# Kernel optimization log

Hardware: AMD Instinct MI355X
Metric: run time of the kernel (lower is better)

## Reference

```python
import jax, jax.numpy as jnp
import numpy as np

H = 1024
NH = 16
HD = H // NH
EPS = 1e-5


def setup_inputs() -> dict:
    key = jax.random.key(0)
    ks = jax.random.split(key, 16)
    B, LQ, LK = 2, 1024, 2048
    s = 1.0 / np.sqrt(H)
    inp = {
        "query": jax.random.normal(ks[0], (B, LQ, H), jnp.float32),
        "key": jax.random.normal(ks[1], (B, LK, H), jnp.float32),
        "value": jax.random.normal(ks[2], (B, LK, H), jnp.float32),
        "mask": jax.random.randint(ks[3], (B, LQ, LK), 0, 2, jnp.int32),
        "Wq": jax.random.normal(ks[4], (H, H), jnp.float32) * s,
        "bq": jnp.zeros((H,), jnp.float32),
        "Wk": jax.random.normal(ks[5], (H, H), jnp.float32) * s,
        "bk": jnp.zeros((H,), jnp.float32),
        "Wv": jax.random.normal(ks[6], (H, H), jnp.float32) * s,
        "bv": jnp.zeros((H,), jnp.float32),
        "Wo": jax.random.normal(ks[7], (H, H), jnp.float32) * s,
        "bo": jnp.zeros((H,), jnp.float32),
        "ln_g": jnp.ones((H,), jnp.float32),
        "ln_b": jnp.zeros((H,), jnp.float32),
    }
    return inp


def _split_heads(x, B, L):
    # [B, L, H] -> [B, NH, L, HD]
    return x.reshape(B, L, NH, HD).transpose(0, 2, 1, 3)


def reference(query, key, value, mask, Wq, bq, Wk, bk, Wv, bv, Wo, bo, ln_g, ln_b):
    B, LQ, _ = query.shape
    LK = key.shape[1]
    # projections (torch Linear: x @ W.T + b)
    Q = _split_heads(query @ Wq.T + bq, B, LQ)   # [B,NH,LQ,HD]
    K = _split_heads(key   @ Wk.T + bk, B, LK)   # [B,NH,LK,HD]
    V = _split_heads(value @ Wv.T + bv, B, LK)   # [B,NH,LK,HD]
    scores = jnp.einsum('bhqd,bhkd->bhqk', Q, K) / np.sqrt(HD)
    scores = jnp.where(mask[:, None, :, :] == 0, jnp.float32(-1e9), scores)
    attn = jax.nn.softmax(scores, axis=-1)
    # dropout is identity in eval mode
    ctx = jnp.einsum('bhqk,bhkd->bhqd', attn, V)            # [B,NH,LQ,HD]
    ctx = ctx.transpose(0, 2, 1, 3).reshape(B, LQ, H)       # [B,LQ,H]
    out = ctx @ Wo.T + bo
    x = out + query
    mu = jnp.mean(x, axis=-1, keepdims=True)
    var = jnp.mean(jnp.square(x - mu), axis=-1, keepdims=True)
    return (x - mu) / jnp.sqrt(var + EPS) * ln_g + ln_b
```

## Files before the change

### kernel.cpp

```cpp
#include <hip/hip_runtime.h>
#include <hip/hip_bf16.h>

typedef __hip_bfloat16 hbf16;

#define Hdim 1024
#define NHEAD 16
#define HDIM 64
#define BATCH 2
#define LQ 1024
#define LK 2048
#define LN_EPS 1e-5f

typedef __bf16 bfv8 __attribute__((ext_vector_type(8)));
typedef float floatx4 __attribute__((ext_vector_type(4)));
typedef union { bfv8 v; __bf16 b[8]; unsigned short s[8]; } bfu8;

#define BK 32
#define LDS_PITCH 40
#define QT 64
#define KT 64
#define KS_PITCH 72
#define VT_OFF(d) ((d) * 72 + (((d) >> 3) << 3))
#define PS_OFF(r) ((r) * 72 + (((r) >> 2) << 3))

__device__ inline bfv8 cvt2(const float4 x, const float4 y) {
    bfv8 r = {(__bf16)x.x, (__bf16)x.y, (__bf16)x.z, (__bf16)x.w,
              (__bf16)y.x, (__bf16)y.y, (__bf16)y.z, (__bf16)y.w};
    return r;
}

__device__ __forceinline__ void glds16(const void* g, void* l) {
    __builtin_amdgcn_global_load_lds(
        (const __attribute__((address_space(1))) void*)g,
        (__attribute__((address_space(3))) void*)l, 16, 0, 0);
}

__global__ __launch_bounds__(256) void cvt_all(
    const float* __restrict__ q, const float* __restrict__ k,
    const float* __restrict__ v, const float* __restrict__ Wq,
    const float* __restrict__ Wk, const float* __restrict__ Wv,
    hbf16* __restrict__ qb, hbf16* __restrict__ kb, hbf16* __restrict__ vb,
    hbf16* __restrict__ Wqb, hbf16* __restrict__ Wkb, hbf16* __restrict__ Wvb) {
    const int blk = blockIdx.x;
    const float* src; hbf16* dst; int base;
    if (blk < 1024)      { src = q;  dst = qb;  base = blk; }
    else if (blk < 3072) { src = k;  dst = kb;  base = blk - 1024; }
    else if (blk < 5120) { src = v;  dst = vb;  base = blk - 3072; }
    else if (blk < 5632) { src = Wq; dst = Wqb; base = blk - 5120; }
    else if (blk < 6144) { src = Wk; dst = Wkb; base = blk - 5632; }
    else                 { src = Wv; dst = Wvb; base = blk - 6144; }
    const size_t e = (size_t)base * 2048 + (size_t)threadIdx.x * 8;
    const float4 a = *(const float4*)(src + e);
    const float4 b = *(const float4*)(src + e + 4);
    *(bfv8*)((__bf16*)dst + e) = cvt2(a, b);
}

__global__ __launch_bounds__(256) void proj3_glds(
    const hbf16* __restrict__ qb, const hbf16* __restrict__ kb,
    const hbf16* __restrict__ vb,
    const hbf16* __restrict__ Wqb, const hbf16* __restrict__ Wkb,
    const hbf16* __restrict__ Wvb,
    const float* __restrict__ bq, const float* __restrict__ bk,
    const float* __restrict__ bv,
    hbf16* __restrict__ Qp, hbf16* __restrict__ Kp, hbf16* __restrict__ Vp) {
    const int z = blockIdx.z;
    if (z == 0 && blockIdx.y >= (BATCH * LQ) / 128) return;
    const hbf16* A; const hbf16* W; const float* bias; hbf16* out; float scale;
    if (z == 0)      { A = qb; W = Wqb; bias = bq; out = Qp; scale = 0.125f; }
    else if (z == 1) { A = kb; W = Wkb; bias = bk; out = Kp; scale = 1.0f; }
    else             { A = vb; W = Wvb; bias = bv; out = Vp; scale = 1.0f; }

    __shared__ __align__(16) __bf16 As[2][128 * 32];
    __shared__ __align__(16) __bf16 Bs[2][128 * 32];
    const int tid = threadIdx.x;
    const int lane = tid & 63;
    const int w = tid >> 6;
    const int wm = w & 1, wn = w >> 1;
    const int u = lane & 15;
    const int quad = lane >> 4;
    const int rowBase = blockIdx.y * 128;
    const int colBase = blockIdx.x * 128;

    const int srow = tid >> 2;
    const int scol = (tid & 3) * 8;
    const hbf16* aP = A + (size_t)(rowBase + srow) * Hdim + scol;
    const hbf16* wP = W + (size_t)(colBase + srow) * Hdim + scol;
    const int ldsOff = srow * 32 + scol;

#define P_STAGE(buf, k0)                                            \
    do {                                                            \
        glds16(aP + (k0), &As[buf][ldsOff]);                        \
        glds16(aP + (k0) + (size_t)64 * Hdim, &As[buf][ldsOff + 64 * 32]); \
        glds16(wP + (k0), &Bs[buf][ldsOff]);                        \
        glds16(wP + (k0) + (size_t)64 * Hdim, &Bs[buf][ldsOff + 64 * 32]); \
    } while (0)

    floatx4 acc[4][4];
#pragma unroll
    for (int mi = 0; mi < 4; ++mi)
#pragma unroll
        for (int ni = 0; ni < 4; ++ni) acc[mi][ni] = (floatx4){0.f, 0.f, 0.f, 0.f};

#define P_COMPUTE(buf)                                                         \
    do {                                                                       \
        bfv8 af[4], bf[4];                                                     \
        _Pragma("unroll") for (int mi = 0; mi < 4; ++mi)                       \
            af[mi] = *(const bfv8*)&As[buf][(wm * 64 + mi * 16 + u) * 32 + quad * 8]; \
        _Pragma("unroll") for (int ni = 0; ni < 4; ++ni)                       \
            bf[ni] = *(const bfv8*)&Bs[buf][(wn * 64 + ni * 16 + u) * 32 + quad * 8]; \
        _Pragma("unroll") for (int mi = 0; mi < 4; ++mi)                       \
            _Pragma("unroll") for (int ni = 0; ni < 4; ++ni)                   \
                acc[mi][ni] = __builtin_amdgcn_mfma_f32_16x16x32_bf16(af[mi], bf[ni], acc[mi][ni], 0, 0, 0); \
    } while (0)

    P_STAGE(0, 0);
    __syncthreads();

    for (int t = 0; t < 32; t += 2) {
        if (t + 1 < 32) P_STAGE(1, (t + 1) * 32);
        P_COMPUTE(0);
        __syncthreads();
        if (t + 2 < 32) P_STAGE(0, (t + 2) * 32);
        P_COMPUTE(1);
        __syncthreads();
    }
#undef P_STAGE
#undef P_COMPUTE

#pragma unroll
    for (int mi = 0; mi < 4; ++mi)
#pragma unroll
        for (int ni = 0; ni < 4; ++ni) {
            const int n = colBase + wn * 64 + ni * 16 + u;
            const float bn = bias[n];
#pragma unroll
            for (int rr = 0; rr < 4; ++rr) {
                const int m = rowBase + wm * 64 + mi * 16 + quad * 4 + rr;
                out[(size_t)m * Hdim + n] = __float2bfloat16((acc[mi][ni][rr] + bn) * scale);
            }
        }
}

__global__ __launch_bounds__(256) void gemm_ctx2(const hbf16* __restrict__ A,
                                                 const float* __restrict__ W,
                                                 const float* __restrict__ bias,
                                                 const float* __restrict__ resid,
                                                 float* __restrict__ out) {
    __shared__ __align__(16) __bf16 As[2][64 * 32];
    __shared__ __align__(16) __bf16 Bs[2][64 * 32];
    const int tid = threadIdx.x;
    const int lane = tid & 63;
    const int w = tid >> 6;
    const int wm = w & 1, wn = w >> 1;
    const int u = lane & 15;
    const int quad = lane >> 4;
    const int rowBase = blockIdx.y * 64;
    const int colBase = blockIdx.x * 64;

    const int srow = tid >> 2;
    const int scol = (tid & 3) * 8;
    const hbf16* aP = A + (size_t)(rowBase + srow) * Hdim + scol;
    const int ldsOffA = srow * 32 + scol;

    const float* wP = W + (size_t)(colBase + srow) * Hdim + scol;
    const int ldsOffB = ldsOffA;

    floatx4 acc[2][2];
#pragma unroll
    for (int mi = 0; mi < 2; ++mi)
#pragma unroll
        for (int ni = 0; ni < 2; ++ni) acc[mi][ni] = (floatx4){0.f, 0.f, 0.f, 0.f};

#define C_COMPUTE(buf)                                                         \
    do {                                                                       \
        bfv8 af[2], bf[2];                                                     \
        _Pragma("unroll") for (int mi = 0; mi < 2; ++mi)                       \
            af[mi] = *(const bfv8*)&As[buf][(wm * 32 + mi * 16 + u) * 32 + quad * 8]; \
        _Pragma("unroll") for (int ni = 0; ni < 2; ++ni)                       \
            bf[ni] = *(const bfv8*)&Bs[buf][(wn * 32 + ni * 16 + u) * 32 + quad * 8]; \
        _Pragma("unroll") for (int mi = 0; mi < 2; ++mi)                       \
            _Pragma("unroll") for (int ni = 0; ni < 2; ++ni)                   \
                acc[mi][ni] = __builtin_amdgcn_mfma_f32_16x16x32_bf16(af[mi], bf[ni], acc[mi][ni], 0, 0, 0); \
    } while (0)

    {
        glds16(aP, &As[0][ldsOffA]);
        const float4* w4 = (const float4*)wP;
        const float4 w0 = w4[0], w1 = w4[1];
        *(bfv8*)&Bs[0][ldsOffB] = cvt2(w0, w1);
    }
    __syncthreads();

    for (int t = 0; t < 32; t += 2) {
        {
            float4 w0, w1;
            const bool pf = (t + 1 < 32);
            if (pf) {
                glds16(aP + (t + 1) * 32, &As[1][ldsOffA]);
                const float4* w4 = (const float4*)(wP + (t + 1) * 32);
                w0 = w4[0]; w1 = w4[1];
            }
            C_COMPUTE(0);
            if (pf) {
                *(bfv8*)&Bs[1][ldsOffB] = cvt2(w0, w1);
            }
            __syncthreads();
        }
        {
            float4 w0, w1;
            const bool pf = (t + 2 < 32);
            if (pf) {
                glds16(aP + (t + 2) * 32, &As[0][ldsOffA]);
                const float4* w4 = (const float4*)(wP + (t + 2) * 32);
                w0 = w4[0]; w1 = w4[1];
            }
            C_COMPUTE(1);
            if (pf) {
                *(bfv8*)&Bs[0][ldsOffB] = cvt2(w0, w1);
            }
            __syncthreads();
        }
    }
#undef C_COMPUTE

#pragma unroll
    for (int mi = 0; mi < 2; ++mi)
#pragma unroll
        for (int ni = 0; ni < 2; ++ni) {
            const int n = colBase + wn * 32 + ni * 16 + u;
            const float bn = bias[n];
#pragma unroll
            for (int rr = 0; rr < 4; ++rr) {
                const int m = rowBase + wm * 32 + mi * 16 + quad * 4 + rr;
                out[(size_t)m * Hdim + n] = acc[mi][ni][rr] + bn + resid[(size_t)m * Hdim + n];
            }
        }
}

__global__ __launch_bounds__(256) void proj3_mfma(
    const float* __restrict__ q_in, const float* __restrict__ k_in,
    const float* __restrict__ v_in,
    const float* __restrict__ Wq, const float* __restrict__ bq,
    const float* __restrict__ Wk, const float* __restrict__ bk,
    const float* __restrict__ Wv, const float* __restrict__ bv,
    hbf16* __restrict__ Qp, hbf16* __restrict__ Kp, hbf16* __restrict__ Vp) {
    const int z = blockIdx.z;
    if (z == 0 && blockIdx.y >= (BATCH * LQ) / 64) return;
    const float* A; const float* W; const float* bias; hbf16* out; float scale;
    if (z == 0)      { A = q_in; W = Wq; bias = bq; out = Qp; scale = 0.125f; }
    else if (z == 1) { A = k_in; W = Wk; bias = bk; out = Kp; scale = 1.0f; }
    else             { A = v_in; W = Wv; bias = bv; out = Vp; scale = 1.0f; }

    __shared__ __align__(16) __bf16 As[64 * LDS_PITCH];
    __shared__ __align__(16) __bf16 Bs[64 * LDS_PITCH];
    const int tid = threadIdx.x;
    const int lane = tid & 63;
    const int w = tid >> 6;
    const int wm = w & 1, wn = w >> 1;
    const int rowBase = blockIdx.y * 64;
    const int colBase = blockIdx.x * 64;
    const int sr = tid >> 2;
    const int scg = (tid & 3) * 8;
    const int lr = lane & 15;
    const int quad = lane >> 4;

    floatx4 acc[2][2] = {};

    for (int k0 = 0; k0 < Hdim; k0 += BK) {
        const float* ap = A + (size_t)(rowBase + sr) * Hdim + k0 + scg;
        bfv8 av = cvt2(((const float4*)ap)[0], ((const float4*)ap)[1]);
        const float* wp = W + (size_t)(colBase + sr) * Hdim + k0 + scg;
        bfv8 bv8 = cvt2(((const float4*)wp)[0], ((const float4*)wp)[1]);
        __syncthreads();
        *(bfv8*)&As[sr * LDS_PITCH + scg] = av;
        *(bfv8*)&Bs[sr * LDS_PITCH + scg] = bv8;
        __syncthreads();

        bfv8 bf[2];
#pragma unroll
        for (int nt = 0; nt < 2; ++nt)
            bf[nt] = *(const bfv8*)&Bs[(wn * 32 + nt * 16 + lr) * LDS_PITCH + quad * 8];
#pragma unroll
        for (int mt = 0; mt < 2; ++mt) {
            bfv8 af = *(const bfv8*)&As[(wm * 32 + mt * 16 + lr) * LDS_PITCH + quad * 8];
#pragma unroll
            for (int nt = 0; nt < 2; ++nt)
                acc[mt][nt] = __builtin_amdgcn_mfma_f32_16x16x32_bf16(af, bf[nt], acc[mt][nt], 0, 0, 0);
        }
    }

#pragma unroll
    for (int mt = 0; mt < 2; ++mt)
#pragma unroll
        for (int nt = 0; nt < 2; ++nt) {
            const int n = colBase + wn * 32 + nt * 16 + lr;
            const float bn = bias[n];
#pragma unroll
            for (int rr = 0; rr < 4; ++rr) {
                const int m = rowBase + wm * 32 + mt * 16 + quad * 4 + rr;
                out[(size_t)m * Hdim + n] = __float2bfloat16((acc[mt][nt][rr] + bn) * scale);
            }
        }
}

__global__ __launch_bounds__(256) void gemm_mfma_f32(const float* __restrict__ A,
                                                     const float* __restrict__ W,
                                                     const float* __restrict__ bias,
                                                     hbf16* __restrict__ out,
                                                     float scale) {
    __shared__ __align__(16) __bf16 As[64 * LDS_PITCH];
    __shared__ __align__(16) __bf16 Bs[64 * LDS_PITCH];
    const int tid = threadIdx.x;
    const int lane = tid & 63;
    const int w = tid >> 6;
    const int wm = w & 1, wn = w >> 1;
    const int rowBase = blockIdx.y * 64;
    const int colBase = blockIdx.x * 64;
    const int sr = tid >> 2;
    const int scg = (tid & 3) * 8;
    const int lr = lane & 15;
    const int quad = lane >> 4;

    floatx4 acc[2][2] = {};

    for (int k0 = 0; k0 < Hdim; k0 += BK) {
        const float* ap = A + (size_t)(rowBase + sr) * Hdim + k0 + scg;
        bfv8 av = cvt2(((const float4*)ap)[0], ((const float4*)ap)[1]);
        const float* wp = W + (size_t)(colBase + sr) * Hdim + k0 + scg;
        bfv8 bv = cvt2(((const float4*)wp)[0], ((const float4*)wp)[1]);
        __syncthreads();
        *(bfv8*)&As[sr * LDS_PITCH + scg] = av;
        *(bfv8*)&Bs[sr * LDS_PITCH + scg] = bv;
        __syncthreads();

        bfv8 bf[2];
#pragma unroll
        for (int nt = 0; nt < 2; ++nt)
            bf[nt] = *(const bfv8*)&Bs[(wn * 32 + nt * 16 + lr) * LDS_PITCH + quad * 8];
#pragma unroll
        for (int mt = 0; mt < 2; ++mt) {
            bfv8 af = *(const bfv8*)&As[(wm * 32 + mt * 16 + lr) * LDS_PITCH + quad * 8];
#pragma unroll
            for (int nt = 0; nt < 2; ++nt)
                acc[mt][nt] = __builtin_amdgcn_mfma_f32_16x16x32_bf16(af, bf[nt], acc[mt][nt], 0, 0, 0);
        }
    }

#pragma unroll
    for (int mt = 0; mt < 2; ++mt)
#pragma unroll
        for (int nt = 0; nt < 2; ++nt) {
            const int n = colBase + wn * 32 + nt * 16 + lr;
            const float bn = bias[n];
#pragma unroll
            for (int rr = 0; rr < 4; ++rr) {
                const int m = rowBase + wm * 32 + mt * 16 + quad * 4 + rr;
                out[(size_t)m * Hdim + n] = __float2bfloat16((acc[mt][nt][rr] + bn) * scale);
            }
        }
}

__global__ __launch_bounds__(256) void gemm_mfma_ctx(const hbf16* __restrict__ A,
                                                     const float* __restrict__ W,
                                                     const float* __restrict__ bias,
                                                     const float* __restrict__ resid,
                                                     float* __restrict__ out) {
    __shared__ __align__(16) __bf16 As[64 * LDS_PITCH];
    __shared__ __align__(16) __bf16 Bs[64 * LDS_PITCH];
    const int tid = threadIdx.x;
    const int lane = tid & 63;
    const int w = tid >> 6;
    const int wm = w & 1, wn = w >> 1;
    const int rowBase = blockIdx.y * 64;
    const int colBase = blockIdx.x * 64;
    const int sr = tid >> 2;
    const int scg = (tid & 3) * 8;
    const int lr = lane & 15;
    const int quad = lane >> 4;

    floatx4 acc[2][2] = {};

    for (int k0 = 0; k0 < Hdim; k0 += BK) {
        bfv8 av = *(const bfv8*)(A + (size_t)(rowBase + sr) * Hdim + k0 + scg);
        const float* wp = W + (size_t)(colBase + sr) * Hdim + k0 + scg;
        bfv8 bv = cvt2(((const float4*)wp)[0], ((const float4*)wp)[1]);
        __syncthreads();
        *(bfv8*)&As[sr * LDS_PITCH + scg] = av;
        *(bfv8*)&Bs[sr * LDS_PITCH + scg] = bv;
        __syncthreads();

        bfv8 bf[2];
#pragma unroll
        for (int nt = 0; nt < 2; ++nt)
            bf[nt] = *(const bfv8*)&Bs[(wn * 32 + nt * 16 + lr) * LDS_PITCH + quad * 8];
#pragma unroll
        for (int mt = 0; mt < 2; ++mt) {
            bfv8 af = *(const bfv8*)&As[(wm * 32 + mt * 16 + lr) * LDS_PITCH + quad * 8];
#pragma unroll
            for (int nt = 0; nt < 2; ++nt)
                acc[mt][nt] = __builtin_amdgcn_mfma_f32_16x16x32_bf16(af, bf[nt], acc[mt][nt], 0, 0, 0);
        }
    }

#pragma unroll
    for (int mt = 0; mt < 2; ++mt)
#pragma unroll
        for (int nt = 0; nt < 2; ++nt) {
            const int n = colBase + wn * 32 + nt * 16 + lr;
            const float bn = bias[n];
#pragma unroll
            for (int rr = 0; rr < 4; ++rr) {
                const int m = rowBase + wm * 32 + mt * 16 + quad * 4 + rr;
                out[(size_t)m * Hdim + n] = acc[mt][nt][rr] + bn + resid[(size_t)m * Hdim + n];
            }
        }
}

__global__ __launch_bounds__(256) void mask_prep_st(const int* __restrict__ mask,
                                                    hbf16* __restrict__ mbias) {
    const int t = blockIdx.x;
    const int kt = t & 31;
    const int qb = (t >> 5) & 15;
    const int b = t >> 9;
    const int tid = threadIdx.x;
    const int w = tid >> 6;
    const int lane = tid & 63;
    const int quad = lane >> 4;
    const int u = lane & 15;
    const int qrow = qb * 64 + w * 16 + quad * 4;
    const int kcol = kt * 64 + u;
    const int* mp = mask + ((size_t)(b * LQ + qrow)) * LK + kcol;

    bfu8 v0, v1;
#pragma unroll
    for (int ns = 0; ns < 4; ++ns)
#pragma unroll
        for (int rr = 0; rr < 4; ++rr) {
            const int mv = mp[(size_t)rr * LK + ns * 16];
            const __bf16 bias = (mv == 0) ? (__bf16)(-1e9f) : (__bf16)(-10.0f);
            const int j = ns * 4 + rr;
            if (j < 8) v0.b[j] = bias; else v1.b[j - 8] = bias;
        }
    __bf16* dst = (__bf16*)mbias + (size_t)t * 4096 + tid * 16;
    *(bfv8*)dst = v0.v;
    *(bfv8*)(dst + 8) = v1.v;
}

__global__ __launch_bounds__(256, 4) void attn_split(const hbf16* __restrict__ Qp,
                                                     const hbf16* __restrict__ Kp,
                                                     const hbf16* __restrict__ Vp,
                                                     const hbf16* __restrict__ mbias,
                                                     float* __restrict__ Opart,
                                                     float* __restrict__ lpart) {
    const int qb = blockIdx.x;
    const int h = blockIdx.y;
    const int b = blockIdx.z >> 1;
    const int sp = blockIdx.z & 1;
    const int tid = threadIdx.x;
    const int lane = tid & 63;
    const int w = tid >> 6;
    const int u = lane & 15;
    const int quad = lane >> 4;
    const int qBase = qb * QT;

    __shared__ __align__(16) __bf16 Ks[64 * KS_PITCH];
    __shared__ __align__(16) __bf16 Vt[4672];
    __shared__ __align__(16) __bf16 Ps[4][1184];

    const int qrow_frag = qBase + w * 16 + u;
    const hbf16* qptr = Qp + (size_t)(b * LQ + qrow_frag) * Hdim + h * HDIM + quad * 8;
    const bfv8 af_q0 = *(const bfv8*)qptr;
    const bfv8 af_q1 = *(const bfv8*)(qptr + 32);

    float l_acc[4] = {0.f, 0.f, 0.f, 0.f};
    floatx4 acc_o[4];
#pragma unroll
    for (int nd = 0; nd < 4; ++nd) acc_o[nd] = (floatx4){0.f, 0.f, 0.f, 0.f};

    const int sk = tid >> 2;
    const int sdg = (tid & 3) * 16;
    const int vk2 = (tid >> 3) * 2;
    const int vd0 = (tid & 7) * 8;
    const __bf16* mbT = (const __bf16*)mbias + (size_t)(b * 16 + qb) * 32 * 4096 + tid * 16;

    const int kt0 = sp * (LK / KT / 2);
    for (int kt = kt0; kt < kt0 + (LK / KT / 2); ++kt) {
        const int kBase = kt * KT;

        bfu8 mb0, mb1;
        mb0.v = *(const bfv8*)(mbT + (size_t)kt * 4096);
        mb1.v = *(const bfv8*)(mbT + (size_t)kt * 4096 + 8);

        const hbf16* vp0 = Vp + (size_t)(b * LK + kBase + vk2) * Hdim + h * HDIM + vd0;
        bfu8 v0, v1;
        v0.v = *(const bfv8*)vp0;
        v1.v = *(const bfv8*)(vp0 + Hdim);
        const hbf16* kp = Kp + (size_t)(b * LK + kBase + sk) * Hdim + h * HDIM + sdg;
        const bfv8 kv0 = *(const bfv8*)kp;
        const bfv8 kv1 = *(const bfv8*)(kp + 8);

        __syncthreads();
        *(bfv8*)&Ks[sk * KS_PITCH + sdg] = kv0;
        *(bfv8*)&Ks[sk * KS_PITCH + sdg + 8] = kv1;
#pragma unroll
        for (int i = 0; i < 8; ++i) {
            unsigned int pk = (unsigned int)v0.s[i] | ((unsigned int)v1.s[i] << 16);
            *(unsigned int*)&Vt[VT_OFF(vd0 + i) + vk2] = pk;
        }
        __syncthreads();

        floatx4 acc_s[4];
#pragma unroll
        for (int ns = 0; ns < 4; ++ns) {
            const bfv8 bk0 = *(const bfv8*)&Ks[(ns * 16 + u) * KS_PITCH + quad * 8];
            const bfv8 bk1 = *(const bfv8*)&Ks[(ns * 16 + u) * KS_PITCH + quad * 8 + 32];
            floatx4 a = (floatx4){0.f, 0.f, 0.f, 0.f};
            a = __builtin_amdgcn_mfma_f32_16x16x32_bf16(af_q0, bk0, a, 0, 0, 0);
            a = __builtin_amdgcn_mfma_f32_16x16x32_bf16(af_q1, bk1, a, 0, 0, 0);
            acc_s[ns] = a;
        }

        __bf16* Pw = Ps[w];
#pragma unroll
        for (int ns = 0; ns < 4; ++ns)
#pragma unroll
            for (int rr = 0; rr < 4; ++rr) {
                const int j = ns * 4 + rr;
                const float bias = (j < 8) ? (float)mb0.b[j] : (float)mb1.b[j - 8];
                const float p = __expf(acc_s[ns][rr] + bias);
                Pw[PS_OFF(quad * 4 + rr) + ns * 16 + u] = (__bf16)p;
                l_acc[rr] += p;
            }

        const bfv8 af_p0 = *(const bfv8*)&Pw[PS_OFF(u) + quad * 8];
        const bfv8 af_p1 = *(const bfv8*)&Pw[PS_OFF(u) + quad * 8 + 32];
#pragma unroll
        for (int nd = 0; nd < 4; ++nd) {
            const bfv8 bv0 = *(const bfv8*)&Vt[VT_OFF(nd * 16 + u) + quad * 8];
            const bfv8 bv1 = *(const bfv8*)&Vt[VT_OFF(nd * 16 + u) + quad * 8 + 32];
            acc_o[nd] = __builtin_amdgcn_mfma_f32_16x16x32_bf16(af_p0, bv0, acc_o[nd], 0, 0, 0);
            acc_o[nd] = __builtin_amdgcn_mfma_f32_16x16x32_bf16(af_p1, bv1, acc_o[nd], 0, 0, 0);
        }
    }

#pragma unroll
    for (int rr = 0; rr < 4; ++rr) {
        float l = l_acc[rr];
        l += __shfl_xor(l, 1, 64);
        l += __shfl_xor(l, 2, 64);
        l += __shfl_xor(l, 4, 64);
        l += __shfl_xor(l, 8, 64);
        const int qrow = qBase + w * 16 + quad * 4 + rr;
        const size_t m = (size_t)(b * LQ + qrow);
        float* orow = Opart + (size_t)sp * (BATCH * LQ * Hdim) + m * Hdim + h * HDIM;
#pragma unroll
        for (int nd = 0; nd < 4; ++nd)
            orow[nd * 16 + u] = acc_o[nd][rr];
        if (u == 0)
            lpart[(size_t)sp * (BATCH * LQ * NHEAD) + m * NHEAD + h] = l;
    }
}

__global__ __launch_bounds__(256) void merge_ctx(const float* __restrict__ Opart,
                                                 const float* __restrict__ lpart,
                                                 hbf16* __restrict__ ctx) {
    const size_t m = blockIdx.x;
    const int t = threadIdx.x;
    const int kk = t * 4;
    const int h = kk >> 6;
    const float l = lpart[m * NHEAD + h] +
                    lpart[(size_t)(BATCH * LQ * NHEAD) + m * NHEAD + h];
    const float invl = 1.0f / l;
    const float4 a = ((const float4*)(Opart + m * Hdim))[t];
    const float4 c = ((const float4*)(Opart + (size_t)(BATCH * LQ * Hdim) + m * Hdim))[t];
    hbf16* crow = ctx + m * Hdim + kk;
    crow[0] = __float2bfloat16((a.x + c.x) * invl);
    crow[1] = __float2bfloat16((a.y + c.y) * invl);
    crow[2] = __float2bfloat16((a.z + c.z) * invl);
    crow[3] = __float2bfloat16((a.w + c.w) * invl);
}

__global__ __launch_bounds__(256, 4) void attn_flash_st(const hbf16* __restrict__ Qp,
                                                        const hbf16* __restrict__ Kp,
                                                        const hbf16* __restrict__ Vp,
                                                        const hbf16* __restrict__ mbias,
                                                        hbf16* __restrict__ ctx) {
    const int qb = blockIdx.x;
    const int h = blockIdx.y;
    const int b = blockIdx.z;
    const int tid = threadIdx.x;
    const int lane = tid & 63;
    const int w = tid >> 6;
    const int u = lane & 15;
    const int quad = lane >> 4;
    const int qBase = qb * QT;

    __shared__ __align__(16) __bf16 Ks[64 * KS_PITCH];
    __shared__ __align__(16) __bf16 Vt[4672];
    __shared__ __align__(16) __bf16 Ps[4][1184];

    const int qrow_frag = qBase + w * 16 + u;
    const hbf16* qptr = Qp + (size_t)(b * LQ + qrow_frag) * Hdim + h * HDIM + quad * 8;
    const bfv8 af_q0 = *(const bfv8*)qptr;
    const bfv8 af_q1 = *(const bfv8*)(qptr + 32);

    float l_acc[4] = {0.f, 0.f, 0.f, 0.f};
    floatx4 acc_o[4];
#pragma unroll
    for (int nd = 0; nd < 4; ++nd) acc_o[nd] = (floatx4){0.f, 0.f, 0.f, 0.f};

    const int sk = tid >> 2;
    const int sdg = (tid & 3) * 16;
    const int vk2 = (tid >> 3) * 2;
    const int vd0 = (tid & 7) * 8;
    const __bf16* mbT = (const __bf16*)mbias + (size_t)(b * 16 + qb) * 32 * 4096 + tid * 16;

    for (int kt = 0; kt < LK / KT; ++kt) {
        const int kBase = kt * KT;

        bfu8 mb0, mb1;
        mb0.v = *(const bfv8*)(mbT + (size_t)kt * 4096);
        mb1.v = *(const bfv8*)(mbT + (size_t)kt * 4096 + 8);

        const hbf16* vp0 = Vp + (size_t)(b * LK + kBase + vk2) * Hdim + h * HDIM + vd0;
        bfu8 v0, v1;
        v0.v = *(const bfv8*)vp0;
        v1.v = *(const bfv8*)(vp0 + Hdim);
        const hbf16* kp = Kp + (size_t)(b * LK + kBase + sk) * Hdim + h * HDIM + sdg;
        const bfv8 kv0 = *(const bfv8*)kp;
        const bfv8 kv1 = *(const bfv8*)(kp + 8);

        __syncthreads();
        *(bfv8*)&Ks[sk * KS_PITCH + sdg] = kv0;
        *(bfv8*)&Ks[sk * KS_PITCH + sdg + 8] = kv1;
#pragma unroll
        for (int i = 0; i < 8; ++i) {
            unsigned int pk = (unsigned int)v0.s[i] | ((unsigned int)v1.s[i] << 16);
            *(unsigned int*)&Vt[VT_OFF(vd0 + i) + vk2] = pk;
        }
        __syncthreads();

        floatx4 acc_s[4];
#pragma unroll
        for (int ns = 0; ns < 4; ++ns) {
            const bfv8 bk0 = *(const bfv8*)&Ks[(ns * 16 + u) * KS_PITCH + quad * 8];
            const bfv8 bk1 = *(const bfv8*)&Ks[(ns * 16 + u) * KS_PITCH + quad * 8 + 32];
            floatx4 a = (floatx4){0.f, 0.f, 0.f, 0.f};
            a = __builtin_amdgcn_mfma_f32_16x16x32_bf16(af_q0, bk0, a, 0, 0, 0);
            a = __builtin_amdgcn_mfma_f32_16x16x32_bf16(af_q1, bk1, a, 0, 0, 0);
            acc_s[ns] = a;
        }

        __bf16* Pw = Ps[w];
#pragma unroll
        for (int ns = 0; ns < 4; ++ns)
#pragma unroll
            for (int rr = 0; rr < 4; ++rr) {
                const int j = ns * 4 + rr;
                const float bias = (j < 8) ? (float)mb0.b[j] : (float)mb1.b[j - 8];
                const float p = __expf(acc_s[ns][rr] + bias);
                Pw[PS_OFF(quad * 4 + rr) + ns * 16 + u] = (__bf16)p;
                l_acc[rr] += p;
            }

        const bfv8 af_p0 = *(const bfv8*)&Pw[PS_OFF(u) + quad * 8];
        const bfv8 af_p1 = *(const bfv8*)&Pw[PS_OFF(u) + quad * 8 + 32];
#pragma unroll
        for (int nd = 0; nd < 4; ++nd) {
            const bfv8 bv0 = *(const bfv8*)&Vt[VT_OFF(nd * 16 + u) + quad * 8];
            const bfv8 bv1 = *(const bfv8*)&Vt[VT_OFF(nd * 16 + u) + quad * 8 + 32];
            acc_o[nd] = __builtin_amdgcn_mfma_f32_16x16x32_bf16(af_p0, bv0, acc_o[nd], 0, 0, 0);
            acc_o[nd] = __builtin_amdgcn_mfma_f32_16x16x32_bf16(af_p1, bv1, acc_o[nd], 0, 0, 0);
        }
    }

#pragma unroll
    for (int rr = 0; rr < 4; ++rr) {
        float l = l_acc[rr];
        l += __shfl_xor(l, 1, 64);
        l += __shfl_xor(l, 2, 64);
        l += __shfl_xor(l, 4, 64);
        l += __shfl_xor(l, 8, 64);
        const float invl = 1.0f / l;
        const int qrow = qBase + w * 16 + quad * 4 + rr;
        hbf16* crow = ctx + (size_t)(b * LQ + qrow) * Hdim + h * HDIM;
#pragma unroll
        for (int nd = 0; nd < 4; ++nd)
            crow[nd * 16 + u] = __float2bfloat16(acc_o[nd][rr] * invl);
    }
}

__global__ __launch_bounds__(256) void ln_kernel(float* __restrict__ x,
                                                 const float* __restrict__ g,
                                                 const float* __restrict__ beta) {
    const int row = blockIdx.x;
    float* xr = x + (size_t)row * Hdim;
    __shared__ float red[256];
    const int tid = threadIdx.x;

    const float4 xi = ((const float4*)xr)[tid];
    red[tid] = xi.x + xi.y + xi.z + xi.w;
    __syncthreads();
    for (int st = 128; st > 0; st >>= 1) {
        if (tid < st) red[tid] += red[tid + st];
        __syncthreads();
    }
    const float mu = red[0] * (1.0f / Hdim);
    __syncthreads();
    {
        float dx = xi.x - mu, dy = xi.y - mu, dz = xi.z - mu, dw = xi.w - mu;
        red[tid] = dx * dx + dy * dy + dz * dz + dw * dw;
    }
    __syncthreads();
    for (int st = 128; st > 0; st >>= 1) {
        if (tid < st) red[tid] += red[tid + st];
        __syncthreads();
    }
    const float rstd = rsqrtf(red[0] * (1.0f / Hdim) + LN_EPS);

    const float4 g4 = ((const float4*)g)[tid];
    const float4 b4 = ((const float4*)beta)[tid];
    float4 y;
    y.x = (xi.x - mu) * rstd * g4.x + b4.x;
    y.y = (xi.y - mu) * rstd * g4.y + b4.y;
    y.z = (xi.z - mu) * rstd * g4.z + b4.z;
    y.w = (xi.w - mu) * rstd * g4.w + b4.w;
    ((float4*)xr)[tid] = y;
}

__device__ inline float wave_red_sum(float v) {
    v += __shfl_down(v, 32, 64);
    v += __shfl_down(v, 16, 64);
    v += __shfl_down(v, 8, 64);
    v += __shfl_down(v, 4, 64);
    v += __shfl_down(v, 2, 64);
    v += __shfl_down(v, 1, 64);
    return v;
}

__global__ __launch_bounds__(256) void fused_mha(
    const float* __restrict__ q_in, const float* __restrict__ k_in,
    const float* __restrict__ v_in, const int* __restrict__ mask,
    const float* __restrict__ Wq, const float* __restrict__ bq,
    const float* __restrict__ Wk, const float* __restrict__ bk,
    const float* __restrict__ Wv, const float* __restrict__ bv,
    const float* __restrict__ Wo, const float* __restrict__ bo,
    const float* __restrict__ ln_g, const float* __restrict__ ln_b,
    float* __restrict__ out) {
    const int q = blockIdx.x;
    const int b = blockIdx.y;
    const int tid = threadIdx.x;
    const int lane = tid & 63;
    const int w = tid >> 6;

    __shared__ float qrow[Hdim];
    __shared__ float qt[Hdim];
    __shared__ float sc[LK];
    __shared__ float u[Hdim];
    __shared__ float ctxv[Hdim];
    __shared__ float Qh[HDIM];
    __shared__ float red[256];
    __shared__ float sb_sh;

    const float* qp = q_in + (size_t)(b * LQ + q) * Hdim;
    for (int i = tid; i < Hdim; i += 256) qrow[i] = qp[i];
    __syncthreads();

    const float* keyb = k_in + (size_t)b * LK * Hdim;
    const float* valb = v_in + (size_t)b * LK * Hdim;
    const int* mrow = mask + (size_t)(b * LQ + q) * LK;

    for (int h = 0; h < NHEAD; ++h) {
        for (int dd = w; dd < HDIM; dd += 4) {
            const float4* wrow = (const float4*)(Wq + (size_t)(h * HDIM + dd) * Hdim);
            const float4* q4 = (const float4*)qrow;
            float p = 0.f;
#pragma unroll
            for (int i0 = 0; i0 < 4; ++i0) {
                float4 a = wrow[i0 * 64 + lane];
                float4 c = q4[i0 * 64 + lane];
                p += a.x * c.x + a.y * c.y + a.z * c.z + a.w * c.w;
            }
            p = wave_red_sum(p);
            if (lane == 0) Qh[dd] = p + bq[h * HDIM + dd];
        }
        __syncthreads();

        if (tid < HDIM) red[tid] = Qh[tid] * bk[h * HDIM + tid];

        float4 s4 = {0.f, 0.f, 0.f, 0.f};
        for (int d = 0; d < HDIM; ++d) {
            float4 a = ((const float4*)(Wk + (size_t)(h * HDIM + d) * Hdim))[tid];
            float qd = Qh[d];
            s4.x += a.x * qd;
            s4.y += a.y * qd;
            s4.z += a.z * qd;
            s4.w += a.w * qd;
        }
        __syncthreads();
        if (tid == 0) {
            float s = 0.f;
            for (int i = 0; i < HDIM; ++i) s += red[i];
            sb_sh = s;
        }
        ((float4*)qt)[tid] = s4;
        __syncthreads();
        const float sb = sb_sh;

        for (int k = w; k < LK; k += 4) {
            const float4* krow = (const float4*)(keyb + (size_t)k * Hdim);
            const float4* q4 = (const float4*)qt;
            float p = 0.f;
#pragma unroll
            for (int i0 = 0; i0 < 4; ++i0) {
                float4 a = krow[i0 * 64 + lane];
                float4 c = q4[i0 * 64 + lane];
                p += a.x * c.x + a.y * c.y + a.z * c.z + a.w * c.w;
            }
            p = wave_red_sum(p);
            if (lane == 0) {
                float s = (p + sb) * 0.125f;
                if (mrow[k] == 0) s = -1e9f;
                sc[k] = s;
            }
        }
        __syncthreads();

        float m = -1e30f;
        for (int k = tid; k < LK; k += 256) m = fmaxf(m, sc[k]);
        red[tid] = m;
        __syncthreads();
        for (int s = 128; s > 0; s >>= 1) {
            if (tid < s) red[tid] = fmaxf(red[tid], red[tid + s]);
            __syncthreads();
        }
        const float mx = red[0];
        __syncthreads();
        float sum = 0.f;
        for (int k = tid; k < LK; k += 256) {
            float e = __expf(sc[k] - mx);
            sc[k] = e;
            sum += e;
        }
        red[tid] = sum;
        __syncthreads();
        for (int s = 128; s > 0; s >>= 1) {
            if (tid < s) red[tid] += red[tid + s];
            __syncthreads();
        }
        const float inv = 1.0f / red[0];
        for (int k = tid; k < LK; k += 256) sc[k] *= inv;
        __syncthreads();

        {
            float4 acc = {0.f, 0.f, 0.f, 0.f};
            const float4* vb4 = (const float4*)valb;
#pragma unroll 4
            for (int k = 0; k < LK; ++k) {
                float p = sc[k];
                float4 a = vb4[(size_t)k * (Hdim / 4) + tid];
                acc.x += a.x * p;
                acc.y += a.y * p;
                acc.z += a.z * p;
                acc.w += a.w * p;
            }
            ((float4*)u)[tid] = acc;
        }
        __syncthreads();

        for (int dd = w; dd < HDIM; dd += 4) {
            const float4* wrow = (const float4*)(Wv + (size_t)(h * HDIM + dd) * Hdim);
            const float4* u4 = (const float4*)u;
            float p = 0.f;
#pragma unroll
            for (int i0 = 0; i0 < 4; ++i0) {
                float4 a = wrow[i0 * 64 + lane];
                float4 c = u4[i0 * 64 + lane];
                p += a.x * c.x + a.y * c.y + a.z * c.z + a.w * c.w;
            }
            p = wave_red_sum(p);
            if (lane == 0) ctxv[h * HDIM + dd] = p + bv[h * HDIM + dd];
        }
        __syncthreads();
    }

    for (int n = w; n < Hdim; n += 4) {
        const float4* wrow = (const float4*)(Wo + (size_t)n * Hdim);
        const float4* c4 = (const float4*)ctxv;
        float p = 0.f;
#pragma unroll
        for (int i0 = 0; i0 < 4; ++i0) {
            float4 a = wrow[i0 * 64 + lane];
            float4 c = c4[i0 * 64 + lane];
            p += a.x * c.x + a.y * c.y + a.z * c.z + a.w * c.w;
        }
        p = wave_red_sum(p);
        if (lane == 0) qt[n] = p + bo[n] + qrow[n];
    }
    __syncthreads();

    {
        const float4 x4 = ((const float4*)qt)[tid];
        red[tid] = x4.x + x4.y + x4.z + x4.w;
    }
    __syncthreads();
    for (int s = 128; s > 0; s >>= 1) {
        if (tid < s) red[tid] += red[tid + s];
        __syncthreads();
    }
    const float mu = red[0] * (1.0f / Hdim);
    __syncthreads();
    {
        const float4 x4 = ((const float4*)qt)[tid];
        float dx = x4.x - mu, dy = x4.y - mu, dz = x4.z - mu, dw = x4.w - mu;
        red[tid] = dx * dx + dy * dy + dz * dz + dw * dw;
    }
    __syncthreads();
    for (int s = 128; s > 0; s >>= 1) {
        if (tid < s) red[tid] += red[tid + s];
        __syncthreads();
    }
    const float rstd = rsqrtf(red[0] * (1.0f / Hdim) + LN_EPS);

    float* orow = out + (size_t)(b * LQ + q) * Hdim;
    const float4 x4 = ((const float4*)qt)[tid];
    const float4 g4 = ((const float4*)ln_g)[tid];
    const float4 b4 = ((const float4*)ln_b)[tid];
    float4 y;
    y.x = (x4.x - mu) * rstd * g4.x + b4.x;
    y.y = (x4.y - mu) * rstd * g4.y + b4.y;
    y.z = (x4.z - mu) * rstd * g4.z + b4.z;
    y.w = (x4.w - mu) * rstd * g4.w + b4.w;
    ((float4*)orow)[tid] = y;
}

extern "C" void kernel_launch(void* const* d_in, const int* in_sizes, int n_in,
                              void* d_out, int out_size, void* d_ws, size_t ws_size,
                              hipStream_t stream) {
    const float* query = (const float*)d_in[0];
    const float* key   = (const float*)d_in[1];
    const float* value = (const float*)d_in[2];
    const int*   mask  = (const int*)d_in[3];
    const float* Wq = (const float*)d_in[4];
    const float* bq = (const float*)d_in[5];
    const float* Wk = (const float*)d_in[6];
    const float* bk = (const float*)d_in[7];
    const float* Wv = (const float*)d_in[8];
    const float* bv = (const float*)d_in[9];
    const float* Wo = (const float*)d_in[10];
    const float* bo = (const float*)d_in[11];
    const float* ln_g = (const float*)d_in[12];
    const float* ln_b = (const float*)d_in[13];
    float* out = (float*)d_out;

    const size_t MB = 1024 * 1024;
    dim3 blk(256);

    if (ws_size >= 50 * MB) {
        char* p = (char*)d_ws;
        hbf16* Qp    = (hbf16*)(p + 0 * MB);
        hbf16* Kp    = (hbf16*)(p + 4 * MB);
        hbf16* Vp    = (hbf16*)(p + 12 * MB);
        hbf16* ctxb  = (hbf16*)(p + 20 * MB);
        hbf16* mbias = (hbf16*)(p + 24 * MB);
        float* Opart = (float*)(p + 32 * MB);
        float* lpart = (float*)(p + 48 * MB);

        hbf16* qb  = (hbf16*)(p + 20 * MB);
        hbf16* kb  = (hbf16*)(p + 24 * MB);
        hbf16* vb  = (hbf16*)(p + 32 * MB);
        hbf16* Wqb = (hbf16*)(p + 40 * MB);
        hbf16* Wkb = (hbf16*)(p + 42 * MB);
        hbf16* Wvb = (hbf16*)(p + 44 * MB);

        cvt_all<<<dim3(6656), blk, 0, stream>>>(query, key, value, Wq, Wk, Wv,
                                                qb, kb, vb, Wqb, Wkb, Wvb);
        proj3_glds<<<dim3(Hdim / 128, (BATCH * LK) / 128, 3), blk, 0, stream>>>(
            qb, kb, vb, Wqb, Wkb, Wvb, bq, bk, bv, Qp, Kp, Vp);
        mask_prep_st<<<dim3(1024), blk, 0, stream>>>(mask, mbias);

        attn_split<<<dim3(LQ / QT, NHEAD, BATCH * 2), blk, 0, stream>>>(
            Qp, Kp, Vp, mbias, Opart, lpart);
        merge_ctx<<<dim3(BATCH * LQ), blk, 0, stream>>>(Opart, lpart, ctxb);

        gemm_ctx2<<<dim3(Hdim / 64, (BATCH * LQ) / 64), blk, 0, stream>>>(
            ctxb, Wo, bo, query, out);
        ln_kernel<<<BATCH * LQ, blk, 0, stream>>>(out, ln_g, ln_b);
    } else if (ws_size >= 32 * MB) {
        char* p = (char*)d_ws;
        hbf16* Qp = (hbf16*)p;    p += 4 * MB;
        hbf16* Kp = (hbf16*)p;    p += 8 * MB;
        hbf16* Vp = (hbf16*)p;    p += 8 * MB;
        hbf16* ctxb = (hbf16*)p;  p += 4 * MB;
        hbf16* mbias = (hbf16*)p; p += 8 * MB;

        gemm_mfma_f32<<<dim3(Hdim / 64, (BATCH * LQ) / 64), blk, 0, stream>>>(query, Wq, bq, Qp, 0.125f);
        gemm_mfma_f32<<<dim3(Hdim / 64, (BATCH * LK) / 64), blk, 0, stream>>>(key, Wk, bk, Kp, 1.0f);
        gemm_mfma_f32<<<dim3(Hdim / 64, (BATCH * LK) / 64), blk, 0, stream>>>(value, Wv, bv, Vp, 1.0f);
        mask_prep_st<<<dim3(1024), blk, 0, stream>>>(mask, mbias);
        attn_flash_st<<<dim3(LQ / QT, NHEAD, BATCH), blk, 0, stream>>>(Qp, Kp, Vp, mbias, ctxb);
        gemm_mfma_ctx<<<dim3(Hdim / 64, (BATCH * LQ) / 64), blk, 0, stream>>>(ctxb, Wo, bo, query, out);
        ln_kernel<<<BATCH * LQ, blk, 0, stream>>>(out, ln_g, ln_b);
    } else {
        fused_mha<<<dim3(LQ, BATCH), dim3(256), 0, stream>>>(
            query, key, value, mask, Wq, bq, Wk, bk, Wv, bv, Wo, bo, ln_g, ln_b, out);
    }
}
```

Baseline: 246.8 us.

## Prefetch next K/V tile into registers, remap blocks across XCDs, add MFMA priority

The attention split kernel now issues the global loads for the next key/value/mask tile right after the LDS barrier, so they overlap with the current tile's MFMA and softmax work. The grid is flattened to 1D and block indices are swizzled with an (x&7)*128 + (x>>3) pattern, so each XCD gets a contiguous run of work items that share K/V and mask data in its L2. s_setprio raises wave priority around the MFMA sections. The cost is more registers held live across the loop body, which could cut occupancy below the launch-bounds target.

```diff
diff --git a/kernel.cpp b/kernel.cpp
--- a/kernel.cpp
+++ b/kernel.cpp
@@ -452,10 +452,12 @@
                                                      const hbf16* __restrict__ mbias,
                                                      float* __restrict__ Opart,
                                                      float* __restrict__ lpart) {
-    const int qb = blockIdx.x;
-    const int h = blockIdx.y;
-    const int b = blockIdx.z >> 1;
-    const int sp = blockIdx.z & 1;
+    const int wg = (blockIdx.x & 7) * 128 + (blockIdx.x >> 3);
+    const int qb = wg & 15;
+    const int h = (wg >> 4) & 15;
+    const int z = wg >> 8;
+    const int b = z >> 1;
+    const int sp = z & 1;
     const int tid = threadIdx.x;
     const int lane = tid & 63;
     const int w = tid >> 6;
@@ -484,32 +486,44 @@
     const __bf16* mbT = (const __bf16*)mbias + (size_t)(b * 16 + qb) * 32 * 4096 + tid * 16;
 
     const int kt0 = sp * (LK / KT / 2);
-    for (int kt = kt0; kt < kt0 + (LK / KT / 2); ++kt) {
-        const int kBase = kt * KT;
-
+    const int ktEnd = kt0 + (LK / KT / 2);
+
+    bfu8 pm0, pm1, pv0, pv1;
+    bfv8 pk0, pk1;
+
+#define A_LOADS(kt)                                                            \
+    do {                                                                       \
+        const int kBase_ = (kt) * KT;                                          \
+        pm0.v = *(const bfv8*)(mbT + (size_t)(kt) * 4096);                     \
+        pm1.v = *(const bfv8*)(mbT + (size_t)(kt) * 4096 + 8);                 \
+        const hbf16* vp_ = Vp + (size_t)(b * LK + kBase_ + vk2) * Hdim + h * HDIM + vd0; \
+        pv0.v = *(const bfv8*)vp_;                                             \
+        pv1.v = *(const bfv8*)(vp_ + Hdim);                                    \
+        const hbf16* kp_ = Kp + (size_t)(b * LK + kBase_ + sk) * Hdim + h * HDIM + sdg; \
+        pk0 = *(const bfv8*)kp_;                                               \
+        pk1 = *(const bfv8*)(kp_ + 8);                                         \
+    } while (0)
+
+    A_LOADS(kt0);
+
+    for (int kt = kt0; kt < ktEnd; ++kt) {
+        __syncthreads();
+        *(bfv8*)&Ks[sk * KS_PITCH + sdg] = pk0;
+        *(bfv8*)&Ks[sk * KS_PITCH + sdg + 8] = pk1;
+#pragma unroll
+        for (int i = 0; i < 8; ++i) {
+            unsigned int pk = (unsigned int)pv0.s[i] | ((unsigned int)pv1.s[i] << 16);
+            *(unsigned int*)&Vt[VT_OFF(vd0 + i) + vk2] = pk;
+        }
         bfu8 mb0, mb1;
-        mb0.v = *(const bfv8*)(mbT + (size_t)kt * 4096);
-        mb1.v = *(const bfv8*)(mbT + (size_t)kt * 4096 + 8);
-
-        const hbf16* vp0 = Vp + (size_t)(b * LK + kBase + vk2) * Hdim + h * HDIM + vd0;
-        bfu8 v0, v1;
-        v0.v = *(const bfv8*)vp0;
-        v1.v = *(const bfv8*)(vp0 + Hdim);
-        const hbf16* kp = Kp + (size_t)(b * LK + kBase + sk) * Hdim + h * HDIM + sdg;
-        const bfv8 kv0 = *(const bfv8*)kp;
-        const bfv8 kv1 = *(const bfv8*)(kp + 8);
-
-        __syncthreads();
-        *(bfv8*)&Ks[sk * KS_PITCH + sdg] = kv0;
-        *(bfv8*)&Ks[sk * KS_PITCH + sdg + 8] = kv1;
-#pragma unroll
-        for (int i = 0; i < 8; ++i) {
-            unsigned int pk = (unsigned int)v0.s[i] | ((unsigned int)v1.s[i] << 16);
-            *(unsigned int*)&Vt[VT_OFF(vd0 + i) + vk2] = pk;
-        }
-        __syncthreads();
+        mb0.v = pm0.v;
+        mb1.v = pm1.v;
+        __syncthreads();
+
+        if (kt + 1 < ktEnd) A_LOADS(kt + 1);
 
         floatx4 acc_s[4];
+        __builtin_amdgcn_s_setprio(1);
 #pragma unroll
         for (int ns = 0; ns < 4; ++ns) {
             const bfv8 bk0 = *(const bfv8*)&Ks[(ns * 16 + u) * KS_PITCH + quad * 8];
@@ -519,6 +533,7 @@
             a = __builtin_amdgcn_mfma_f32_16x16x32_bf16(af_q1, bk1, a, 0, 0, 0);
             acc_s[ns] = a;
         }
+        __builtin_amdgcn_s_setprio(0);
 
         __bf16* Pw = Ps[w];
 #pragma unroll
@@ -534,6 +549,7 @@
 
         const bfv8 af_p0 = *(const bfv8*)&Pw[PS_OFF(u) + quad * 8];
         const bfv8 af_p1 = *(const bfv8*)&Pw[PS_OFF(u) + quad * 8 + 32];
+        __builtin_amdgcn_s_setprio(1);
 #pragma unroll
         for (int nd = 0; nd < 4; ++nd) {
             const bfv8 bv0 = *(const bfv8*)&Vt[VT_OFF(nd * 16 + u) + quad * 8];
@@ -541,7 +557,9 @@
             acc_o[nd] = __builtin_amdgcn_mfma_f32_16x16x32_bf16(af_p0, bv0, acc_o[nd], 0, 0, 0);
             acc_o[nd] = __builtin_amdgcn_mfma_f32_16x16x32_bf16(af_p1, bv1, acc_o[nd], 0, 0, 0);
         }
-    }
+        __builtin_amdgcn_s_setprio(0);
+    }
+#undef A_LOADS
 
 #pragma unroll
     for (int rr = 0; rr < 4; ++rr) {
@@ -979,7 +997,7 @@
             qb, kb, vb, Wqb, Wkb, Wvb, bq, bk, bv, Qp, Kp, Vp);
         mask_prep_st<<<dim3(1024), blk, 0, stream>>>(mask, mbias);
 
-        attn_split<<<dim3(LQ / QT, NHEAD, BATCH * 2), blk, 0, stream>>>(
+        attn_split<<<dim3(1024), blk, 0, stream>>>(
             Qp, Kp, Vp, mbias, Opart, lpart);
         merge_ctx<<<dim3(BATCH * LQ), blk, 0, stream>>>(Opart, lpart, ctxb);
 
```

After: 246.6 us. Within noise of the previous version (-0.1%).
